# Kernel optimization log

Hardware: AMD Instinct MI355X
Metric: run time of the kernel (lower is better)

Reference implementation:

```python
import jax, jax.numpy as jnp
import numpy as np

LAYER_NUMBER = 1  # coeff for query_key_layer_scaling; cancels mathematically
HEAD_DIM = 128

def setup_inputs() -> dict:
    key = jax.random.key(0)
    k1, k2, k3, k4 = jax.random.split(key, 4)
    s, b, h, d = 2048, 2, 16, HEAD_DIM
    return {
        "query_layer": jax.random.normal(k1, (s, b, h, d), dtype=jnp.float32),
        "key_layer": jax.random.normal(k2, (s, b, h, d), dtype=jnp.float32),
        "value_layer": jax.random.normal(k3, (s, b, h, d), dtype=jnp.float32),
        "attention_mask": jax.random.randint(k4, (b, 1, s, s), 0, 2).astype(jnp.bool_),
    }

def reference(query_layer, key_layer, value_layer, attention_mask):
    s, b, h, d = query_layer.shape
    # norm_factor = sqrt(d) * layer_number; softmax scale (coeff) = layer_number
    norm_factor = jnp.sqrt(jnp.asarray(d, jnp.float32)) * LAYER_NUMBER
    coeff = jnp.asarray(LAYER_NUMBER, jnp.float32)
    # raw scores [b, h, sq, sk]
    scores = jnp.einsum('sbhd,tbhd->bhst', query_layer, key_layer) / norm_factor
    # fused scale-mask-softmax, in fp32 (attention_softmax_in_fp32=True)
    scores32 = scores.astype(jnp.float32) * coeff
    scores32 = jnp.where(attention_mask, jnp.float32(-10000.0), scores32)
    probs = jax.nn.softmax(scores32, axis=-1).astype(query_layer.dtype)
    # dropout p=0.0 -> identity
    # context: [b, h, sq, d] -> [sq, b, h*d]
    ctx = jnp.einsum('bhst,tbhd->sbhd', probs, value_layer)
    return ctx.reshape(s, b, h * d)
```

## Files before the change

kernel.cpp:

```cpp
#include <hip/hip_runtime.h>
#include <hip/hip_bf16.h>

#define S_LEN 2048
#define NB 2
#define NH 16
#define DH 128
#define ROW_STRIDE (NB * NH * DH)
#define M_TILE 128
#define N_TILE 64
#define NKT (S_LEN / N_TILE)
#define NWORDS (NB * S_LEN * (S_LEN / 64))

typedef __bf16 bf16x8_t __attribute__((ext_vector_type(8)));
typedef __bf16 bf16x4_t __attribute__((ext_vector_type(4)));
typedef float  f32x4_t  __attribute__((ext_vector_type(4)));

#define AS1 __attribute__((address_space(1)))
#define AS3 __attribute__((address_space(3)))

__device__ __forceinline__ void gload_lds16(const void* g, void* l) {
    __builtin_amdgcn_global_load_lds((const AS1 void*)g, (AS3 void*)l, 16, 0, 0);
}

__device__ __forceinline__ float vexp2(float x) {
    float r;
    asm("v_exp_f32 %0, %1" : "=v"(r) : "v"(x));
    return r;
}
__device__ __forceinline__ unsigned vcvtpk(float a, float b) {
    unsigned r;
    asm("v_cvt_pk_bf16_f32 %0, %1, %2" : "=v"(r) : "v"(a), "v"(b));
    return r;
}

template <int CTRL>
__device__ __forceinline__ float dppmov(float x) {
    return __builtin_bit_cast(float,
        __builtin_amdgcn_update_dpp(0, __builtin_bit_cast(int, x), CTRL, 0xF, 0xF, true));
}
__device__ __forceinline__ float rowmax16(float x) {
    x = fmaxf(x, dppmov<0xB1>(x));
    x = fmaxf(x, dppmov<0x4E>(x));
    x = fmaxf(x, dppmov<0x141>(x));
    x = fmaxf(x, dppmov<0x140>(x));
    return x;
}
__device__ __forceinline__ float rowsum16(float x) {
    x += dppmov<0xB1>(x);
    x += dppmov<0x4E>(x);
    x += dppmov<0x141>(x);
    x += dppmov<0x140>(x);
    return x;
}

__global__ __launch_bounds__(256) void prep_kernel(
    const float* __restrict__ Kg, const float* __restrict__ Vg,
    const int* __restrict__ Mg,
    __bf16* __restrict__ Kb, __bf16* __restrict__ Vb,
    unsigned long long* __restrict__ Wg)
{
    __shared__ float tf[64][129];
    const int tid = threadIdx.x;
    const int blk = blockIdx.x;

    if (blk < 1024) {
        const int bh = blk >> 5;
        const int kt = blk & 31;
        const int b = bh >> 4, h = bh & (NH - 1);
        const int head_off = b * (NH * DH) + h * DH;
        char* tile = (char*)Kb + (size_t)blk * 16384;
#pragma unroll
        for (int it = 0; it < 4; ++it) {
            const int idx = it * 256 + tid;
            const int tl = idx >> 4;
            const int d8 = (idx & 15) * 8;
            const float* src = Kg + (size_t)(kt * 64 + tl) * ROW_STRIDE + head_off + d8;
            float4 f0 = *(const float4*)src;
            float4 f1 = *(const float4*)(src + 4);
            bf16x8_t v;
            v[0] = (__bf16)f0.x; v[1] = (__bf16)f0.y; v[2] = (__bf16)f0.z; v[3] = (__bf16)f0.w;
            v[4] = (__bf16)f1.x; v[5] = (__bf16)f1.y; v[6] = (__bf16)f1.z; v[7] = (__bf16)f1.w;
            *(bf16x8_t*)(tile + tl * 256 + ((d8 * 2) ^ ((tl & 7) << 4))) = v;
        }
    } else if (blk < 2048) {
        const int vb = blk - 1024;
        const int bh = vb >> 5;
        const int kt = vb & 31;
        const int b = bh >> 4, h = bh & (NH - 1);
        const int head_off = b * (NH * DH) + h * DH;
        char* tile = (char*)Vb + (size_t)vb * 16384;
#pragma unroll
        for (int i = 0; i < 8; ++i) {
            int idx = i * 256 + tid;
            int t  = idx >> 5;
            int d4 = (idx & 31) * 4;
            float4 f = *(const float4*)(Vg + (size_t)(kt * 64 + t) * ROW_STRIDE + head_off + d4);
            tf[t][d4 + 0] = f.x; tf[t][d4 + 1] = f.y;
            tf[t][d4 + 2] = f.z; tf[t][d4 + 3] = f.w;
        }
        __syncthreads();
#pragma unroll
        for (int i = 0; i < 8; ++i) {
            int idx = i * 256 + tid;
            int d  = idx >> 4;
            int t4 = (idx & 15) * 4;
            bf16x4_t w;
            w[0] = (__bf16)tf[t4 + 0][d];
            w[1] = (__bf16)tf[t4 + 1][d];
            w[2] = (__bf16)tf[t4 + 2][d];
            w[3] = (__bf16)tf[t4 + 3][d];
            const int col = (t4 & 32) * 2 + ((t4 >> 2) & 3) * 16 + ((t4 & 16) >> 1);
            *(bf16x4_t*)(tile + d * 128 + (col ^ ((d & 7) << 4))) = w;
        }
    } else {
        const int lane = tid & 63;
        const int wv = ((blk - 2048) * 256 + tid) >> 6;
#pragma unroll
        for (int i = 0; i < 16; ++i) {
            const int wid = wv * 16 + i;
            const int v = Mg[(size_t)wid * 64 + lane];
            const unsigned long long bal = __ballot(v != 0);
            if (lane == 0) Wg[wid] = bal;
        }
    }
}

__global__ __launch_bounds__(256) void mask_pack(
    const int* __restrict__ Mg, unsigned long long* __restrict__ Wg)
{
    const int lane = threadIdx.x & 63;
    const int wv = (blockIdx.x * blockDim.x + threadIdx.x) >> 6;
#pragma unroll
    for (int i = 0; i < 4; ++i) {
        const int wid = wv * 4 + i;
        const int v = Mg[(size_t)wid * 64 + lane];
        const unsigned long long bal = __ballot(v != 0);
        if (lane == 0) Wg[wid] = bal;
    }
}

__global__ __launch_bounds__(512, 4) void fa_kernel(
    const float* __restrict__ Qg, const __bf16* __restrict__ Kb,
    const __bf16* __restrict__ Vb, const unsigned long long* __restrict__ Mw,
    float* __restrict__ Og)
{
    __shared__ __bf16 kT[2][64 * 128];
    __shared__ __bf16 vT[2][128 * 64];

    const int tid  = threadIdx.x;
    const int wave = tid >> 6;
    const int lane = tid & 63;
    const int l15  = lane & 15;
    const int quad = lane >> 4;
    const int swz  = (l15 & 7) << 4;

    const int bid = blockIdx.x;
    const int lb  = ((bid & 7) << 6) | (bid >> 3);
    const int qt  = lb & 15;
    const int bh  = lb >> 4;
    const int h   = bh & (NH - 1);
    const int b   = bh >> 4;

    const int q0       = qt * M_TILE;
    const int head_off = b * (NH * DH) + h * DH;

    const float kScale = 1.44269504088896340736f / 11.31370849898476039f;

    const uint2* mrow = (const uint2*)Mw
        + (size_t)b * (S_LEN * (S_LEN / 64))
        + (size_t)(q0 + wave * 16) * (S_LEN / 64);

    const char* KbBH = (const char*)Kb + (size_t)bh * (NKT * 16384);
    const char* VbBH = (const char*)Vb + (size_t)bh * (NKT * 16384);

    bf16x8_t qf[4];
    {
        const int srow = q0 + wave * 16 + l15;
        const float* qp = Qg + (size_t)srow * ROW_STRIDE + head_off + quad * 8;
#pragma unroll
        for (int kc = 0; kc < 4; ++kc) {
            float4 f0 = *(const float4*)(qp + kc * 32);
            float4 f1 = *(const float4*)(qp + kc * 32 + 4);
            bf16x8_t v;
            v[0] = (__bf16)(f0.x * kScale); v[1] = (__bf16)(f0.y * kScale);
            v[2] = (__bf16)(f0.z * kScale); v[3] = (__bf16)(f0.w * kScale);
            v[4] = (__bf16)(f1.x * kScale); v[5] = (__bf16)(f1.y * kScale);
            v[6] = (__bf16)(f1.z * kScale); v[7] = (__bf16)(f1.w * kScale);
            qf[kc] = v;
        }
    }

    f32x4_t oacc[8];
    float lsum = 0.0f;
#pragma unroll
    for (int dt = 0; dt < 8; ++dt) oacc[dt] = {0.0f, 0.0f, 0.0f, 0.0f};

    auto STAGE = [&](int buf, int kt_) {
        const char* ks = KbBH + (size_t)kt_ * 16384;
        const char* vs = VbBH + (size_t)kt_ * 16384;
#pragma unroll
        for (int i = 0; i < 2; ++i) {
            const int c = (wave * 2 + i) * 1024;
            gload_lds16(ks + c + lane * 16, (char*)&kT[buf][0] + c);
            gload_lds16(vs + c + lane * 16, (char*)&vT[buf][0] + c);
        }
    };

    STAGE(0, 0);
    asm volatile("s_waitcnt vmcnt(0)" ::: "memory");
    __builtin_amdgcn_s_barrier();
    int cur = 0;

    for (int kt = 0; kt < NKT; ++kt) {
        if (kt + 1 < NKT) STAGE(cur ^ 1, kt + 1);

        const uint2 mwv = mrow[(size_t)l15 * (S_LEN / 64) + kt];

        const char* kbuf = (const char*)&kT[cur][0];
        f32x4_t sacc[4];
#pragma unroll
        for (int n = 0; n < 4; ++n) sacc[n] = {0.0f, 0.0f, 0.0f, 0.0f};
        __builtin_amdgcn_s_setprio(1);
#pragma unroll
        for (int n = 0; n < 4; ++n) {
#pragma unroll
            for (int kc = 0; kc < 4; ++kc) {
                bf16x8_t kb = *(const bf16x8_t*)(kbuf + (n * 16 + l15) * 256
                                                 + ((kc * 64 + quad * 16) ^ swz));
                sacc[n] = __builtin_amdgcn_mfma_f32_16x16x32_bf16(kb, qf[kc], sacc[n], 0, 0, 0);
            }
        }
        __builtin_amdgcn_s_setprio(0);

        unsigned pk[4][2];
        {
            const unsigned ex0 = mwv.x >> (quad * 4);
            const unsigned ex1 = mwv.y >> (quad * 4);
            float p[4][4];
#pragma unroll
            for (int n = 0; n < 4; ++n) {
                const unsigned ex = (n < 2) ? ex0 : ex1;
                const int sh = (n & 1) * 16;
#pragma unroll
                for (int r = 0; r < 4; ++r) {
                    const float e = vexp2(sacc[n][r]);
                    p[n][r] = ((ex >> (sh + r)) & 1u) ? 0.0f : e;
                }
            }
            float s0 = (p[0][0] + p[0][1]) + (p[0][2] + p[0][3]);
            float s1 = (p[1][0] + p[1][1]) + (p[1][2] + p[1][3]);
            float s2 = (p[2][0] + p[2][1]) + (p[2][2] + p[2][3]);
            float s3 = (p[3][0] + p[3][1]) + (p[3][2] + p[3][3]);
            lsum += (s0 + s1) + (s2 + s3);
#pragma unroll
            for (int n = 0; n < 4; ++n) {
                pk[n][0] = vcvtpk(p[n][0], p[n][1]);
                pk[n][1] = vcvtpk(p[n][2], p[n][3]);
            }
        }

        const char* vbuf = (const char*)&vT[cur][0];
        __builtin_amdgcn_s_setprio(1);
#pragma unroll
        for (int kc2 = 0; kc2 < 2; ++kc2) {
            int4 a;
            a.x = (int)pk[2 * kc2][0];
            a.y = (int)pk[2 * kc2][1];
            a.z = (int)pk[2 * kc2 + 1][0];
            a.w = (int)pk[2 * kc2 + 1][1];
            const bf16x8_t af = __builtin_bit_cast(bf16x8_t, a);
#pragma unroll
            for (int dt = 0; dt < 8; ++dt) {
                bf16x8_t bfr = *(const bf16x8_t*)(vbuf + (dt * 16 + l15) * 128
                                                  + ((kc2 * 64 + quad * 16) ^ swz));
                oacc[dt] = __builtin_amdgcn_mfma_f32_16x16x32_bf16(af, bfr, oacc[dt], 0, 0, 0);
            }
        }
        __builtin_amdgcn_s_setprio(0);

        asm volatile("s_waitcnt vmcnt(0)" ::: "memory");
        __builtin_amdgcn_s_barrier();
        cur ^= 1;
    }

    float tot = lsum;
    tot += __shfl_xor(tot, 16, 64);
    tot += __shfl_xor(tot, 32, 64);
#pragma unroll
    for (int r = 0; r < 4; ++r) {
        const float inv = 1.0f / __shfl(tot, quad * 4 + r, 64);
        const int srow = q0 + wave * 16 + quad * 4 + r;
        float* op = Og + (size_t)srow * ROW_STRIDE + head_off + l15;
#pragma unroll
        for (int dt = 0; dt < 8; ++dt) op[dt * 16] = oacc[dt][r] * inv;
    }
}

#define LDS_KS 136
#define LDS_VS 72
#define LDS_PS 68

__global__ __launch_bounds__(256, 2) void fa_kernel_fb(
    const float* __restrict__ Qg, const float* __restrict__ Kg,
    const float* __restrict__ Vg, const unsigned long long* __restrict__ Mw,
    float* __restrict__ Og)
{
    __shared__ __bf16 kT[64 * LDS_KS];
    __shared__ __bf16 vT[DH * LDS_VS];
    __shared__ __bf16 pT[4 * 32 * LDS_PS];

    const int tid  = threadIdx.x;
    const int wave = tid >> 6;
    const int lane = tid & 63;
    const int l15  = lane & 15;
    const int quad = lane >> 4;

    const int bid = blockIdx.x;
    const int qt  = bid & 15;
    const int bh  = bid >> 4;
    const int h   = bh & (NH - 1);
    const int b   = bh >> 4;

    const int q0       = qt * M_TILE;
    const int head_off = b * (NH * DH) + h * DH;

    const float kScale   = 1.44269504088896340736f / 11.31370849898476039f;
    const float kMaskVal = -14426.950408889634f;
    const float kThr     = 8.0f;

    const uint2* mrow = (const uint2*)Mw
        + (size_t)b * (S_LEN * (S_LEN / 64))
        + (size_t)(q0 + wave * 32) * (S_LEN / 64);

    bf16x8_t qf[2][4];
#pragma unroll
    for (int mt = 0; mt < 2; ++mt) {
        const int srow = q0 + wave * 32 + mt * 16 + l15;
        const float* qp = Qg + (size_t)srow * ROW_STRIDE + head_off + quad * 8;
#pragma unroll
        for (int kc = 0; kc < 4; ++kc) {
            float4 f0 = *(const float4*)(qp + kc * 32);
            float4 f1 = *(const float4*)(qp + kc * 32 + 4);
            bf16x8_t v;
            v[0] = (__bf16)f0.x; v[1] = (__bf16)f0.y;
            v[2] = (__bf16)f0.z; v[3] = (__bf16)f0.w;
            v[4] = (__bf16)f1.x; v[5] = (__bf16)f1.y;
            v[6] = (__bf16)f1.z; v[7] = (__bf16)f1.w;
            qf[mt][kc] = v;
        }
    }

    f32x4_t oacc[2][8];
    float mstate[2][4], lstate[2][4];
#pragma unroll
    for (int mt = 0; mt < 2; ++mt) {
#pragma unroll
        for (int dt = 0; dt < 8; ++dt) oacc[mt][dt] = {0.0f, 0.0f, 0.0f, 0.0f};
#pragma unroll
        for (int r = 0; r < 4; ++r) { mstate[mt][r] = -3.0e38f; lstate[mt][r] = 0.0f; }
    }

    __bf16* pW = &pT[wave * 32 * LDS_PS];

    for (int kt = 0; kt < NKT; ++kt) {
        const int t0 = kt * N_TILE;
        __syncthreads();

        {
            const int r0 = tid >> 5;
            const int c4 = (tid & 31) * 4;
            const float* kp = Kg + (size_t)(t0 + r0) * ROW_STRIDE + head_off + c4;
            __bf16* kd = &kT[r0 * LDS_KS + c4];
#pragma unroll
            for (int rr = 0; rr < 8; ++rr) {
                float4 f = *(const float4*)kp;
                bf16x4_t w;
                w[0] = (__bf16)f.x; w[1] = (__bf16)f.y;
                w[2] = (__bf16)f.z; w[3] = (__bf16)f.w;
                *(bf16x4_t*)kd = w;
                kp += 8 * ROW_STRIDE;
                kd += 8 * LDS_KS;
            }
        }
        {
            const int dv = tid & 31;
            const int tg = tid >> 5;
            const float* vbase = Vg + (size_t)(t0 + tg * 8) * ROW_STRIDE + head_off + dv;
#pragma unroll
            for (int j = 0; j < 4; ++j) {
                const int d = dv + j * 32;
#pragma unroll
                for (int tt = 0; tt < 2; ++tt) {
                    const float* vp = vbase + j * 32 + (size_t)(tt * 4) * ROW_STRIDE;
                    bf16x4_t w;
                    w[0] = (__bf16)vp[0 * ROW_STRIDE];
                    w[1] = (__bf16)vp[1 * ROW_STRIDE];
                    w[2] = (__bf16)vp[2 * ROW_STRIDE];
                    w[3] = (__bf16)vp[3 * ROW_STRIDE];
                    *(bf16x4_t*)&vT[d * LDS_VS + tg * 8 + tt * 4] = w;
                }
            }
        }
        __syncthreads();

        uint2 mw[2][4];
#pragma unroll
        for (int mt = 0; mt < 2; ++mt)
#pragma unroll
            for (int r = 0; r < 4; ++r)
                mw[mt][r] = mrow[(size_t)(mt * 16 + quad * 4 + r) * (S_LEN / 64) + kt];

        f32x4_t sacc[2][4];
#pragma unroll
        for (int mt = 0; mt < 2; ++mt)
#pragma unroll
            for (int n = 0; n < 4; ++n) sacc[mt][n] = {0.0f, 0.0f, 0.0f, 0.0f};
#pragma unroll
        for (int n = 0; n < 4; ++n) {
#pragma unroll
            for (int kc = 0; kc < 4; ++kc) {
                bf16x8_t kb = *(const bf16x8_t*)&kT[(n * 16 + l15) * LDS_KS + kc * 32 + quad * 8];
                sacc[0][n] = __builtin_amdgcn_mfma_f32_16x16x32_bf16(qf[0][kc], kb, sacc[0][n], 0, 0, 0);
                sacc[1][n] = __builtin_amdgcn_mfma_f32_16x16x32_bf16(qf[1][kc], kb, sacc[1][n], 0, 0, 0);
            }
        }

#pragma unroll
        for (int mt = 0; mt < 2; ++mt) {
            float sv[4][4];
            float tmv[4];
#pragma unroll
            for (int r = 0; r < 4; ++r) {
                const unsigned a0 = mw[mt][r].x >> l15;
                const unsigned a1 = mw[mt][r].y >> l15;
                sv[0][r] = (a0 & 1u)       ? kMaskVal : sacc[mt][0][r] * kScale;
                sv[1][r] = (a0 & 0x10000u) ? kMaskVal : sacc[mt][1][r] * kScale;
                sv[2][r] = (a1 & 1u)       ? kMaskVal : sacc[mt][2][r] * kScale;
                sv[3][r] = (a1 & 0x10000u) ? kMaskVal : sacc[mt][3][r] * kScale;
                float tm = fmaxf(fmaxf(sv[0][r], sv[1][r]), fmaxf(sv[2][r], sv[3][r]));
                tmv[r] = rowmax16(tm);
            }
            bool need = (tmv[0] > mstate[mt][0] + kThr) |
                        (tmv[1] > mstate[mt][1] + kThr) |
                        (tmv[2] > mstate[mt][2] + kThr) |
                        (tmv[3] > mstate[mt][3] + kThr);
            if (__any(need)) {
#pragma unroll
                for (int r = 0; r < 4; ++r) {
                    const float mold  = mstate[mt][r];
                    const float mnew  = fmaxf(mold, tmv[r]);
                    const float alpha = vexp2(mold - mnew);
                    float rsum = 0.0f;
#pragma unroll
                    for (int n = 0; n < 4; ++n) {
                        float p = vexp2(sv[n][r] - mnew);
                        rsum += p;
                        pW[(mt * 16 + quad * 4 + r) * LDS_PS + n * 16 + l15] = (__bf16)p;
                    }
                    rsum = rowsum16(rsum);
                    lstate[mt][r] = lstate[mt][r] * alpha + rsum;
                    mstate[mt][r] = mnew;
#pragma unroll
                    for (int dt = 0; dt < 8; ++dt) oacc[mt][dt][r] *= alpha;
                }
            } else {
#pragma unroll
                for (int r = 0; r < 4; ++r) {
                    const float mold = mstate[mt][r];
                    float rsum = 0.0f;
#pragma unroll
                    for (int n = 0; n < 4; ++n) {
                        float p = vexp2(sv[n][r] - mold);
                        rsum += p;
                        pW[(mt * 16 + quad * 4 + r) * LDS_PS + n * 16 + l15] = (__bf16)p;
                    }
                    lstate[mt][r] += rowsum16(rsum);
                }
            }
        }

#pragma unroll
        for (int kc2 = 0; kc2 < 2; ++kc2) {
            bf16x8_t af[2];
#pragma unroll
            for (int mt = 0; mt < 2; ++mt) {
                bf16x4_t lo = *(const bf16x4_t*)&pW[(mt * 16 + l15) * LDS_PS + kc2 * 32 + quad * 8];
                bf16x4_t hi = *(const bf16x4_t*)&pW[(mt * 16 + l15) * LDS_PS + kc2 * 32 + quad * 8 + 4];
                af[mt] = __builtin_shufflevector(lo, hi, 0, 1, 2, 3, 4, 5, 6, 7);
            }
#pragma unroll
            for (int dt = 0; dt < 8; ++dt) {
                bf16x8_t bfr = *(const bf16x8_t*)&vT[(dt * 16 + l15) * LDS_VS + kc2 * 32 + quad * 8];
                oacc[0][dt] = __builtin_amdgcn_mfma_f32_16x16x32_bf16(af[0], bfr, oacc[0][dt], 0, 0, 0);
                oacc[1][dt] = __builtin_amdgcn_mfma_f32_16x16x32_bf16(af[1], bfr, oacc[1][dt], 0, 0, 0);
            }
        }
    }

#pragma unroll
    for (int mt = 0; mt < 2; ++mt) {
#pragma unroll
        for (int r = 0; r < 4; ++r) {
            const float inv = 1.0f / lstate[mt][r];
            const int srow = q0 + wave * 32 + mt * 16 + quad * 4 + r;
            float* op = Og + (size_t)srow * ROW_STRIDE + head_off + l15;
#pragma unroll
            for (int dt = 0; dt < 8; ++dt) op[dt * 16] = oacc[mt][dt][r] * inv;
        }
    }
}

extern "C" void kernel_launch(void* const* d_in, const int* in_sizes, int n_in,
                              void* d_out, int out_size, void* d_ws, size_t ws_size,
                              hipStream_t stream) {
    (void)in_sizes; (void)n_in; (void)out_size;
    const float* Q = (const float*)d_in[0];
    const float* K = (const float*)d_in[1];
    const float* V = (const float*)d_in[2];
    const int*   M = (const int*)d_in[3];
    float* O = (float*)d_out;

    const size_t need_fast = ((size_t)33 << 20);

    if (ws_size >= need_fast) {
        __bf16* Kb = (__bf16*)d_ws;
        __bf16* Vb = (__bf16*)((char*)d_ws + ((size_t)16 << 20));
        unsigned long long* Mw = (unsigned long long*)((char*)d_ws + ((size_t)32 << 20));
        hipLaunchKernelGGL(prep_kernel, dim3(4096), dim3(256), 0, stream, K, V, M, Kb, Vb, Mw);
        hipLaunchKernelGGL(fa_kernel, dim3(NB * NH * (S_LEN / M_TILE)), dim3(512), 0, stream,
                           Q, Kb, Vb, Mw, O);
    } else {
        unsigned long long* Mw = (unsigned long long*)d_ws;
        hipLaunchKernelGGL(mask_pack, dim3(NWORDS / 4 * 64 / 256), dim3(256), 0, stream, M, Mw);
        hipLaunchKernelGGL(fa_kernel_fb, dim3(NB * NH * (S_LEN / M_TILE)), dim3(256), 0, stream,
                           Q, K, V, Mw, O);
    }
}
```

Before: 247.5 us.

## Split key tile across wave pairs, each wave computing two query sub-tiles

Reorganizes the 8 waves into 4 query groups by 2 key-column groups. Each wave now covers 32 query rows and 32 keys, so every K and V fragment read from LDS is reused by two MFMAs instead of one, halving LDS read traffic per MFMA. The cost is two extra output accumulator sets per wave, which raises register pressure. A final LDS-based reduction with two extra barriers combines the partial outputs and row sums of the two key groups. No running max is kept, so the split-sum remains exact.

```diff
diff --git a/kernel.cpp b/kernel.cpp
--- a/kernel.cpp
+++ b/kernel.cpp
@@ -64,8 +64,8 @@
     const int blk = blockIdx.x;
 
     if (blk < 1024) {
+        const int kt = blk & 31;
         const int bh = blk >> 5;
-        const int kt = blk & 31;
         const int b = bh >> 4, h = bh & (NH - 1);
         const int head_off = b * (NH * DH) + h * DH;
         char* tile = (char*)Kb + (size_t)blk * 16384;
@@ -144,11 +144,14 @@
     const __bf16* __restrict__ Vb, const unsigned long long* __restrict__ Mw,
     float* __restrict__ Og)
 {
-    __shared__ __bf16 kT[2][64 * 128];
-    __shared__ __bf16 vT[2][128 * 64];
+    __shared__ __align__(16) char smem[65536];
+    char* kTb = smem;
+    char* vTb = smem + 32768;
 
     const int tid  = threadIdx.x;
     const int wave = tid >> 6;
+    const int qg   = wave & 3;
+    const int tg   = wave >> 2;
     const int lane = tid & 63;
     const int l15  = lane & 15;
     const int quad = lane >> 4;
@@ -166,16 +169,17 @@
 
     const float kScale = 1.44269504088896340736f / 11.31370849898476039f;
 
-    const uint2* mrow = (const uint2*)Mw
-        + (size_t)b * (S_LEN * (S_LEN / 64))
-        + (size_t)(q0 + wave * 16) * (S_LEN / 64);
+    const unsigned* mrow32 = (const unsigned*)Mw
+        + ((size_t)b * (S_LEN * (S_LEN / 64))
+           + (size_t)(q0 + qg * 32) * (S_LEN / 64)) * 2 + tg;
 
     const char* KbBH = (const char*)Kb + (size_t)bh * (NKT * 16384);
     const char* VbBH = (const char*)Vb + (size_t)bh * (NKT * 16384);
 
-    bf16x8_t qf[4];
-    {
-        const int srow = q0 + wave * 16 + l15;
+    bf16x8_t qf[2][4];
+#pragma unroll
+    for (int mt = 0; mt < 2; ++mt) {
+        const int srow = q0 + qg * 32 + mt * 16 + l15;
         const float* qp = Qg + (size_t)srow * ROW_STRIDE + head_off + quad * 8;
 #pragma unroll
         for (int kc = 0; kc < 4; ++kc) {
@@ -186,14 +190,18 @@
             v[2] = (__bf16)(f0.z * kScale); v[3] = (__bf16)(f0.w * kScale);
             v[4] = (__bf16)(f1.x * kScale); v[5] = (__bf16)(f1.y * kScale);
             v[6] = (__bf16)(f1.z * kScale); v[7] = (__bf16)(f1.w * kScale);
-            qf[kc] = v;
-        }
-    }
-
-    f32x4_t oacc[8];
-    float lsum = 0.0f;
-#pragma unroll
-    for (int dt = 0; dt < 8; ++dt) oacc[dt] = {0.0f, 0.0f, 0.0f, 0.0f};
+            qf[mt][kc] = v;
+        }
+    }
+
+    f32x4_t oacc[2][8];
+    float lsum[2];
+#pragma unroll
+    for (int mt = 0; mt < 2; ++mt) {
+#pragma unroll
+        for (int dt = 0; dt < 8; ++dt) oacc[mt][dt] = {0.0f, 0.0f, 0.0f, 0.0f};
+        lsum[mt] = 0.0f;
+    }
 
     auto STAGE = [&](int buf, int kt_) {
         const char* ks = KbBH + (size_t)kt_ * 16384;
@@ -201,8 +209,8 @@
 #pragma unroll
         for (int i = 0; i < 2; ++i) {
             const int c = (wave * 2 + i) * 1024;
-            gload_lds16(ks + c + lane * 16, (char*)&kT[buf][0] + c);
-            gload_lds16(vs + c + lane * 16, (char*)&vT[buf][0] + c);
+            gload_lds16(ks + c + lane * 16, kTb + buf * 16384 + c);
+            gload_lds16(vs + c + lane * 16, vTb + buf * 16384 + c);
         }
     };
 
@@ -214,67 +222,67 @@
     for (int kt = 0; kt < NKT; ++kt) {
         if (kt + 1 < NKT) STAGE(cur ^ 1, kt + 1);
 
-        const uint2 mwv = mrow[(size_t)l15 * (S_LEN / 64) + kt];
-
-        const char* kbuf = (const char*)&kT[cur][0];
-        f32x4_t sacc[4];
-#pragma unroll
-        for (int n = 0; n < 4; ++n) sacc[n] = {0.0f, 0.0f, 0.0f, 0.0f};
+        unsigned mword[2];
+#pragma unroll
+        for (int mt = 0; mt < 2; ++mt)
+            mword[mt] = mrow32[((size_t)(mt * 16 + l15) * (S_LEN / 64) + kt) * 2];
+
+        const char* kbuf = kTb + cur * 16384;
+        f32x4_t sacc[2][2];
+#pragma unroll
+        for (int mt = 0; mt < 2; ++mt)
+#pragma unroll
+            for (int n = 0; n < 2; ++n) sacc[mt][n] = {0.0f, 0.0f, 0.0f, 0.0f};
         __builtin_amdgcn_s_setprio(1);
 #pragma unroll
-        for (int n = 0; n < 4; ++n) {
+        for (int n = 0; n < 2; ++n) {
 #pragma unroll
             for (int kc = 0; kc < 4; ++kc) {
-                bf16x8_t kb = *(const bf16x8_t*)(kbuf + (n * 16 + l15) * 256
+                bf16x8_t kb = *(const bf16x8_t*)(kbuf + ((tg * 2 + n) * 16 + l15) * 256
                                                  + ((kc * 64 + quad * 16) ^ swz));
-                sacc[n] = __builtin_amdgcn_mfma_f32_16x16x32_bf16(kb, qf[kc], sacc[n], 0, 0, 0);
+                sacc[0][n] = __builtin_amdgcn_mfma_f32_16x16x32_bf16(kb, qf[0][kc], sacc[0][n], 0, 0, 0);
+                sacc[1][n] = __builtin_amdgcn_mfma_f32_16x16x32_bf16(kb, qf[1][kc], sacc[1][n], 0, 0, 0);
             }
         }
         __builtin_amdgcn_s_setprio(0);
 
-        unsigned pk[4][2];
-        {
-            const unsigned ex0 = mwv.x >> (quad * 4);
-            const unsigned ex1 = mwv.y >> (quad * 4);
-            float p[4][4];
-#pragma unroll
-            for (int n = 0; n < 4; ++n) {
-                const unsigned ex = (n < 2) ? ex0 : ex1;
-                const int sh = (n & 1) * 16;
+        unsigned pk[2][4];
+#pragma unroll
+        for (int mt = 0; mt < 2; ++mt) {
+            const unsigned ex = mword[mt] >> (quad * 4);
+            float p[2][4];
+#pragma unroll
+            for (int n = 0; n < 2; ++n)
 #pragma unroll
                 for (int r = 0; r < 4; ++r) {
-                    const float e = vexp2(sacc[n][r]);
-                    p[n][r] = ((ex >> (sh + r)) & 1u) ? 0.0f : e;
+                    const float e = vexp2(sacc[mt][n][r]);
+                    p[n][r] = ((ex >> (n * 16 + r)) & 1u) ? 0.0f : e;
                 }
-            }
             float s0 = (p[0][0] + p[0][1]) + (p[0][2] + p[0][3]);
             float s1 = (p[1][0] + p[1][1]) + (p[1][2] + p[1][3]);
-            float s2 = (p[2][0] + p[2][1]) + (p[2][2] + p[2][3]);
-            float s3 = (p[3][0] + p[3][1]) + (p[3][2] + p[3][3]);
-            lsum += (s0 + s1) + (s2 + s3);
-#pragma unroll
-            for (int n = 0; n < 4; ++n) {
-                pk[n][0] = vcvtpk(p[n][0], p[n][1]);
-                pk[n][1] = vcvtpk(p[n][2], p[n][3]);
-            }
-        }
-
-        const char* vbuf = (const char*)&vT[cur][0];
+            lsum[mt] += s0 + s1;
+            pk[mt][0] = vcvtpk(p[0][0], p[0][1]);
+            pk[mt][1] = vcvtpk(p[0][2], p[0][3]);
+            pk[mt][2] = vcvtpk(p[1][0], p[1][1]);
+            pk[mt][3] = vcvtpk(p[1][2], p[1][3]);
+        }
+
+        const char* vbuf = vTb + cur * 16384;
+        bf16x8_t af[2];
+#pragma unroll
+        for (int mt = 0; mt < 2; ++mt) {
+            int4 a;
+            a.x = (int)pk[mt][0]; a.y = (int)pk[mt][1];
+            a.z = (int)pk[mt][2]; a.w = (int)pk[mt][3];
+            af[mt] = __builtin_bit_cast(bf16x8_t, a);
+        }
         __builtin_amdgcn_s_setprio(1);
 #pragma unroll
-        for (int kc2 = 0; kc2 < 2; ++kc2) {
-            int4 a;
-            a.x = (int)pk[2 * kc2][0];
-            a.y = (int)pk[2 * kc2][1];
-            a.z = (int)pk[2 * kc2 + 1][0];
-            a.w = (int)pk[2 * kc2 + 1][1];
-            const bf16x8_t af = __builtin_bit_cast(bf16x8_t, a);
-#pragma unroll
-            for (int dt = 0; dt < 8; ++dt) {
-                bf16x8_t bfr = *(const bf16x8_t*)(vbuf + (dt * 16 + l15) * 128
-                                                  + ((kc2 * 64 + quad * 16) ^ swz));
-                oacc[dt] = __builtin_amdgcn_mfma_f32_16x16x32_bf16(af, bfr, oacc[dt], 0, 0, 0);
-            }
+        for (int dt = 0; dt < 8; ++dt) {
+            bf16x8_t bfr = *(const bf16x8_t*)(vbuf + (dt * 16 + l15) * 128
+                                              + ((tg * 64 + quad * 16) ^ swz));
+            oacc[0][dt] = __builtin_amdgcn_mfma_f32_16x16x32_bf16(af[0], bfr, oacc[0][dt], 0, 0, 0);
+            oacc[1][dt] = __builtin_amdgcn_mfma_f32_16x16x32_bf16(af[1], bfr, oacc[1][dt], 0, 0, 0);
         }
         __builtin_amdgcn_s_setprio(0);
 
@@ -283,16 +291,36 @@
         cur ^= 1;
     }
 
-    float tot = lsum;
-    tot += __shfl_xor(tot, 16, 64);
-    tot += __shfl_xor(tot, 32, 64);
-#pragma unroll
-    for (int r = 0; r < 4; ++r) {
-        const float inv = 1.0f / __shfl(tot, quad * 4 + r, 64);
-        const int srow = q0 + wave * 16 + quad * 4 + r;
-        float* op = Og + (size_t)srow * ROW_STRIDE + head_off + l15;
-#pragma unroll
-        for (int dt = 0; dt < 8; ++dt) op[dt * 16] = oacc[dt][r] * inv;
+    float* ob  = (float*)smem;
+    float* lsb = (float*)(smem + 32768);
+#pragma unroll
+    for (int mt = 0; mt < 2; ++mt) {
+        __syncthreads();
+        float tq = lsum[mt];
+        tq += __shfl_xor(tq, 16, 64);
+        tq += __shfl_xor(tq, 32, 64);
+        if (tg == 1) {
+            if (lane < 16) lsb[qg * 16 + l15] = tq;
+#pragma unroll
+            for (int dt = 0; dt < 8; ++dt)
+#pragma unroll
+                for (int r = 0; r < 4; ++r)
+                    ob[(qg * 16 + quad * 4 + r) * 128 + dt * 16 + l15] = oacc[mt][dt][r];
+        }
+        __syncthreads();
+        if (tg == 0) {
+            const float tot = tq + lsb[qg * 16 + l15];
+#pragma unroll
+            for (int r = 0; r < 4; ++r) {
+                const float inv = 1.0f / __shfl(tot, quad * 4 + r, 64);
+                const int srow = q0 + qg * 32 + mt * 16 + quad * 4 + r;
+                float* op = Og + (size_t)srow * ROW_STRIDE + head_off + l15;
+#pragma unroll
+                for (int dt = 0; dt < 8; ++dt)
+                    op[dt * 16] = (oacc[mt][dt][r]
+                                   + ob[(qg * 16 + quad * 4 + r) * 128 + dt * 16 + l15]) * inv;
+            }
+        }
     }
 }
 
@@ -384,8 +412,8 @@
         }
         {
             const int dv = tid & 31;
-            const int tg = tid >> 5;
-            const float* vbase = Vg + (size_t)(t0 + tg * 8) * ROW_STRIDE + head_off + dv;
+            const int tg2 = tid >> 5;
+            const float* vbase = Vg + (size_t)(t0 + tg2 * 8) * ROW_STRIDE + head_off + dv;
 #pragma unroll
             for (int j = 0; j < 4; ++j) {
                 const int d = dv + j * 32;
@@ -397,7 +425,7 @@
                     w[1] = (__bf16)vp[1 * ROW_STRIDE];
                     w[2] = (__bf16)vp[2 * ROW_STRIDE];
                     w[3] = (__bf16)vp[3 * ROW_STRIDE];
-                    *(bf16x4_t*)&vT[d * LDS_VS + tg * 8 + tt * 4] = w;
+                    *(bf16x4_t*)&vT[d * LDS_VS + tg2 * 8 + tt * 4] = w;
                 }
             }
         }
```

After: 301.2 us. 1.22x slower.
